# Optimization experiments

Hardware: AMD Instinct MI355X
Metric: run time of the kernel (lower is better)

The kernel has to match this reference:

```python
import jax, jax.numpy as jnp
import numpy as np

N = 100000   # nodes
E = 1600000  # edges
F = 64       # input node features
H = 64       # hidden dim
G = 512      # graphs in batch


def setup_inputs() -> dict:
    key = jax.random.key(0)
    ks = jax.random.split(key, 10)
    x = jax.random.normal(ks[0], (N, F), dtype=jnp.float32)
    edge_index = jax.random.randint(ks[1], (2, E), 0, N, dtype=jnp.int32)
    batch = jnp.sort(jax.random.randint(ks[2], (N,), 0, G, dtype=jnp.int32))
    s = 1.0 / np.sqrt(H)
    W1 = jax.random.normal(ks[3], (F, H), dtype=jnp.float32) * s
    b1 = jnp.zeros((H,), jnp.float32)
    W2 = jax.random.normal(ks[4], (H, H), dtype=jnp.float32) * s
    b2 = jnp.zeros((H,), jnp.float32)
    W3 = jax.random.normal(ks[5], (H, H), dtype=jnp.float32) * s
    b3 = jnp.zeros((H,), jnp.float32)
    return {"x": x, "edge_index": edge_index, "batch": batch,
            "W1": W1, "b1": b1, "W2": W2, "b2": b2, "W3": W3, "b3": b3}


def _gcn_conv(x, W, b, src, dst, dinv):
    # PyG GCNConv: h = x @ W; aggregate with sym-normalized adjacency incl. self-loops; + bias
    h = x @ W                                  # [N, H]
    norm = dinv[src] * dinv[dst]               # [E]
    agg = jax.ops.segment_sum(h[src] * norm[:, None], dst, num_segments=N)
    agg = agg + h * (dinv * dinv)[:, None]     # self-loop contribution
    return agg + b


def reference(x, edge_index, batch, W1, b1, W2, b2, W3, b3):
    src, dst = edge_index[0], edge_index[1]
    # degree with self-loops (counted on dst, as in PyG)
    deg = jax.ops.segment_sum(jnp.ones((E,), x.dtype), dst, num_segments=N) + 1.0
    dinv = jax.lax.rsqrt(deg)
    h = jax.nn.relu(_gcn_conv(x, W1, b1, src, dst, dinv))
    h = jax.nn.relu(_gcn_conv(h, W2, b2, src, dst, dinv))
    h = _gcn_conv(h, W3, b3, src, dst, dinv)
    # global mean pool over graphs
    sums = jax.ops.segment_sum(h, batch, num_segments=G)          # [G, H]
    cnts = jax.ops.segment_sum(jnp.ones((N,), h.dtype), batch, num_segments=G)
    return sums / jnp.maximum(cnts, 1.0)[:, None]
```

## Files before the change

### kernel.cpp

```cpp
#include <hip/hip_runtime.h>

#define N_NODES 100000
#define N_EDGES 1600000
#define FDIM 64
#define NGRAPH 512
#define NB 782
#define NWG 1024
#define CHUNK 1563
#define DWG 64
#define DCHUNK ((N_NODES + DWG - 1) / DWG)
#define MAXD 128

__device__ __forceinline__ unsigned short f2bf(float v) {
    unsigned int x = __float_as_uint(v);
    x += 0x7FFF + ((x >> 16) & 1);
    return (unsigned short)(x >> 16);
}

__global__ void scan_block(const int* __restrict__ in, int* __restrict__ excl,
                           int* __restrict__ blocksums, int n) {
    __shared__ int lds[256];
    int t = threadIdx.x;
    int base = blockIdx.x * 1024 + t * 4;
    int v0 = (base     < n) ? in[base]     : 0;
    int v1 = (base + 1 < n) ? in[base + 1] : 0;
    int v2 = (base + 2 < n) ? in[base + 2] : 0;
    int v3 = (base + 3 < n) ? in[base + 3] : 0;
    int s = v0 + v1 + v2 + v3;
    lds[t] = s;
    __syncthreads();
    for (int off = 1; off < 256; off <<= 1) {
        int x = (t >= off) ? lds[t - off] : 0;
        __syncthreads();
        lds[t] += x;
        __syncthreads();
    }
    int thrExcl = lds[t] - s;
    if (t == 255) blocksums[blockIdx.x] = lds[255];
    if (base     < n) excl[base]     = thrExcl;
    if (base + 1 < n) excl[base + 1] = thrExcl + v0;
    if (base + 2 < n) excl[base + 2] = thrExcl + v0 + v1;
    if (base + 3 < n) excl[base + 3] = thrExcl + v0 + v1 + v2;
}

__global__ void scan_top2(int* __restrict__ blocksums, int nb, int* __restrict__ out, int n) {
    __shared__ int lds[256];
    int t = threadIdx.x;
    int base = t * 4;
    int v0 = (base     < nb) ? blocksums[base]     : 0;
    int v1 = (base + 1 < nb) ? blocksums[base + 1] : 0;
    int v2 = (base + 2 < nb) ? blocksums[base + 2] : 0;
    int v3 = (base + 3 < nb) ? blocksums[base + 3] : 0;
    int s = v0 + v1 + v2 + v3;
    lds[t] = s;
    __syncthreads();
    for (int off = 1; off < 256; off <<= 1) {
        int x = (t >= off) ? lds[t - off] : 0;
        __syncthreads();
        lds[t] += x;
        __syncthreads();
    }
    int excl = lds[t] - s;
    if (base     < nb) blocksums[base]     = excl;
    if (base + 1 < nb) blocksums[base + 1] = excl + v0;
    if (base + 2 < nb) blocksums[base + 2] = excl + v0 + v1;
    if (base + 3 < nb) blocksums[base + 3] = excl + v0 + v1 + v2;
    if (t == 255) out[n] = lds[255];
}

__global__ void scan_add(int* __restrict__ out, const int* __restrict__ blocksums, int n) {
    int i = blockIdx.x * blockDim.x + threadIdx.x;
    if (i < n) out[i] += blocksums[i >> 10];
}

__global__ __launch_bounds__(256) void hist_kernel(const int* __restrict__ dst,
                                                   int* __restrict__ hist, int E) {
    __shared__ int h[NB];
    int t = threadIdx.x, wg = blockIdx.x;
    for (int i = t; i < NB; i += 256) h[i] = 0;
    __syncthreads();
    int beg = wg * CHUNK, end = min(beg + CHUNK, E);
    for (int i = beg + t; i < end; i += 256) atomicAdd(&h[dst[i] >> 7], 1);
    __syncthreads();
    for (int i = t; i < NB; i += 256) hist[i * NWG + wg] = h[i];
}

__global__ __launch_bounds__(256) void bin_kernel(const int* __restrict__ src,
                                                  const int* __restrict__ dst,
                                                  const int* __restrict__ scannedH,
                                                  int* __restrict__ ebin, int E) {
    __shared__ int base[NB];
    __shared__ int cur[NB];
    int t = threadIdx.x, wg = blockIdx.x;
    for (int i = t; i < NB; i += 256) { base[i] = scannedH[i * NWG + wg]; cur[i] = 0; }
    __syncthreads();
    int beg = wg * CHUNK, end = min(beg + CHUNK, E);
    for (int i = beg + t; i < end; i += 256) {
        int d = dst[i];
        int b = d >> 7;
        int p = base[b] + atomicAdd(&cur[b], 1);
        ebin[p] = ((d & 127) << 17) | src[i];
    }
}

__global__ __launch_bounds__(256) void csr_sort2(const int* __restrict__ ebin,
                                                 const int* __restrict__ scannedH,
                                                 int* __restrict__ csr_src,
                                                 int* __restrict__ offsets,
                                                 float* __restrict__ dinv, int E) {
    __shared__ int cnt[128];
    __shared__ int seg[128];
    __shared__ int cur[128];
    __shared__ int buf[4352];
    int t = threadIdx.x, b = blockIdx.x;
    int nbase = b << 7;
    int nodes = min(128, N_NODES - nbase);
    int bstart = scannedH[b * NWG];
    int bend = (b == NB - 1) ? E : scannedH[(b + 1) * NWG];
    if (t < 128) cnt[t] = 0;
    __syncthreads();
    for (int i = bstart + t; i < bend; i += 256) atomicAdd(&cnt[ebin[i] >> 17], 1);
    __syncthreads();
    if (t < 128) seg[t] = cnt[t];
    __syncthreads();
    for (int off = 1; off < 128; off <<= 1) {
        int v = 0;
        if (t < 128 && t >= off) v = seg[t - off];
        __syncthreads();
        if (t < 128) seg[t] += v;
        __syncthreads();
    }
    if (t < nodes) {
        int excl = seg[t] - cnt[t];
        offsets[nbase + t] = bstart + excl;
        dinv[nbase + t] = rsqrtf((float)cnt[t] + 1.0f);
        cur[t] = excl;
    }
    if (b == 0 && t == 0) offsets[N_NODES] = E;
    __syncthreads();
    for (int i = bstart + t; i < bend; i += 256) {
        int v = ebin[i];
        int p = atomicAdd(&cur[v >> 17], 1);
        buf[p] = v & 0x1FFFF;
    }
    __syncthreads();
    int span = bend - bstart;
    for (int i = t; i < span; i += 256) csr_src[bstart + i] = buf[i];
}

__global__ __launch_bounds__(256) void histD_kernel(const int* __restrict__ offsets,
                                                    int* __restrict__ histD) {
    __shared__ int h[MAXD];
    int t = threadIdx.x, wg = blockIdx.x;
    if (t < MAXD) h[t] = 0;
    __syncthreads();
    int beg = wg * DCHUNK, end = min(beg + DCHUNK, N_NODES);
    for (int i = beg + t; i < end; i += 256) {
        int d = min(offsets[i + 1] - offsets[i], MAXD - 1);
        atomicAdd(&h[d], 1);
    }
    __syncthreads();
    if (t < MAXD) histD[t * DWG + wg] = h[t];
}

__global__ __launch_bounds__(256) void binD_kernel(const int* __restrict__ offsets,
                                                   const int* __restrict__ scannedD,
                                                   int* __restrict__ perm) {
    __shared__ int base[MAXD];
    __shared__ int cur[MAXD];
    int t = threadIdx.x, wg = blockIdx.x;
    if (t < MAXD) { base[t] = scannedD[t * DWG + wg]; cur[t] = 0; }
    __syncthreads();
    int beg = wg * DCHUNK, end = min(beg + DCHUNK, N_NODES);
    for (int i = beg + t; i < end; i += 256) {
        int d = min(offsets[i + 1] - offsets[i], MAXD - 1);
        int pos = base[d] + atomicAdd(&cur[d], 1);
        perm[pos] = i;
    }
}

__global__ __launch_bounds__(256) void gemm64(const float* __restrict__ X,
                                              const float* __restrict__ W,
                                              const float* __restrict__ dinv,
                                              unsigned short* __restrict__ Hout, int n) {
    __shared__ float Ws[64 * 68];
    __shared__ float Xs[64 * 68];
    int t = threadIdx.x;
    int r0 = blockIdx.x * 64;

    #pragma unroll
    for (int kk = 0; kk < 16; ++kk) {
        int idx = t + kk * 256;
        int r = idx >> 6, c = idx & 63;
        Ws[r * 68 + c] = W[idx];
        float v = (r0 + r < n) ? X[(size_t)(r0 + r) * FDIM + c] : 0.0f;
        Xs[c * 68 + r] = v;
    }
    __syncthreads();

    int rg = (t >> 4) << 2;
    int cg = (t & 15) << 2;
    float4 acc0 = {0, 0, 0, 0}, acc1 = {0, 0, 0, 0};
    float4 acc2 = {0, 0, 0, 0}, acc3 = {0, 0, 0, 0};

    #pragma unroll 8
    for (int k = 0; k < 64; ++k) {
        float4 xv = *(const float4*)&Xs[k * 68 + rg];
        float4 wv = *(const float4*)&Ws[k * 68 + cg];
        acc0.x += xv.x * wv.x; acc0.y += xv.x * wv.y; acc0.z += xv.x * wv.z; acc0.w += xv.x * wv.w;
        acc1.x += xv.y * wv.x; acc1.y += xv.y * wv.y; acc1.z += xv.y * wv.z; acc1.w += xv.y * wv.w;
        acc2.x += xv.z * wv.x; acc2.y += xv.z * wv.y; acc2.z += xv.z * wv.z; acc2.w += xv.z * wv.w;
        acc3.x += xv.w * wv.x; acc3.y += xv.w * wv.y; acc3.z += xv.w * wv.z; acc3.w += xv.w * wv.w;
    }

    float4 accs[4] = {acc0, acc1, acc2, acc3};
    #pragma unroll
    for (int i = 0; i < 4; ++i) {
        int row = r0 + rg + i;
        if (row < n) {
            float sc = dinv[row];
            unsigned int u0 = (unsigned int)f2bf(accs[i].x * sc) | ((unsigned int)f2bf(accs[i].y * sc) << 16);
            unsigned int u1 = (unsigned int)f2bf(accs[i].z * sc) | ((unsigned int)f2bf(accs[i].w * sc) << 16);
            *(uint2*)&Hout[(size_t)row * FDIM + cg] = make_uint2(u0, u1);
        }
    }
}

__global__ __launch_bounds__(256) void gather_pn(const unsigned short* __restrict__ hs,
                                                 const int* __restrict__ csr_src,
                                                 const int* __restrict__ offsets,
                                                 const int* __restrict__ perm,
                                                 const float* __restrict__ dinv,
                                                 const float* __restrict__ bias,
                                                 float* __restrict__ outb,
                                                 int n, int do_relu) {
    int slot = (blockIdx.x * 256 + threadIdx.x) >> 3;
    int p = threadIdx.x & 7;
    if (slot >= n) return;
    int node = perm[slot];
    int beg = offsets[node], end = offsets[node + 1];

    float a0 = 0, a1 = 0, a2 = 0, a3 = 0, a4 = 0, a5 = 0, a6 = 0, a7 = 0;
    int k = beg;
    for (; k + 3 < end; k += 4) {
        int s0 = csr_src[k], s1 = csr_src[k + 1], s2 = csr_src[k + 2], s3 = csr_src[k + 3];
        uint4 v0 = *(const uint4*)(hs + ((size_t)s0 << 6) + (p << 3));
        uint4 v1 = *(const uint4*)(hs + ((size_t)s1 << 6) + (p << 3));
        uint4 v2 = *(const uint4*)(hs + ((size_t)s2 << 6) + (p << 3));
        uint4 v3 = *(const uint4*)(hs + ((size_t)s3 << 6) + (p << 3));
        a0 += __uint_as_float(v0.x << 16); a1 += __uint_as_float(v0.x & 0xFFFF0000u);
        a2 += __uint_as_float(v0.y << 16); a3 += __uint_as_float(v0.y & 0xFFFF0000u);
        a4 += __uint_as_float(v0.z << 16); a5 += __uint_as_float(v0.z & 0xFFFF0000u);
        a6 += __uint_as_float(v0.w << 16); a7 += __uint_as_float(v0.w & 0xFFFF0000u);
        a0 += __uint_as_float(v1.x << 16); a1 += __uint_as_float(v1.x & 0xFFFF0000u);
        a2 += __uint_as_float(v1.y << 16); a3 += __uint_as_float(v1.y & 0xFFFF0000u);
        a4 += __uint_as_float(v1.z << 16); a5 += __uint_as_float(v1.z & 0xFFFF0000u);
        a6 += __uint_as_float(v1.w << 16); a7 += __uint_as_float(v1.w & 0xFFFF0000u);
        a0 += __uint_as_float(v2.x << 16); a1 += __uint_as_float(v2.x & 0xFFFF0000u);
        a2 += __uint_as_float(v2.y << 16); a3 += __uint_as_float(v2.y & 0xFFFF0000u);
        a4 += __uint_as_float(v2.z << 16); a5 += __uint_as_float(v2.z & 0xFFFF0000u);
        a6 += __uint_as_float(v2.w << 16); a7 += __uint_as_float(v2.w & 0xFFFF0000u);
        a0 += __uint_as_float(v3.x << 16); a1 += __uint_as_float(v3.x & 0xFFFF0000u);
        a2 += __uint_as_float(v3.y << 16); a3 += __uint_as_float(v3.y & 0xFFFF0000u);
        a4 += __uint_as_float(v3.z << 16); a5 += __uint_as_float(v3.z & 0xFFFF0000u);
        a6 += __uint_as_float(v3.w << 16); a7 += __uint_as_float(v3.w & 0xFFFF0000u);
    }
    for (; k < end; ++k) {
        int s0 = csr_src[k];
        uint4 v0 = *(const uint4*)(hs + ((size_t)s0 << 6) + (p << 3));
        a0 += __uint_as_float(v0.x << 16); a1 += __uint_as_float(v0.x & 0xFFFF0000u);
        a2 += __uint_as_float(v0.y << 16); a3 += __uint_as_float(v0.y & 0xFFFF0000u);
        a4 += __uint_as_float(v0.z << 16); a5 += __uint_as_float(v0.z & 0xFFFF0000u);
        a6 += __uint_as_float(v0.w << 16); a7 += __uint_as_float(v0.w & 0xFFFF0000u);
    }
    uint4 sv = *(const uint4*)(hs + ((size_t)node << 6) + (p << 3));
    float dd = dinv[node];
    int fb = p << 3;
    const float4* bp = (const float4*)(bias + fb);
    float4 bv0 = bp[0], bv1 = bp[1];
    float o0 = dd * (a0 + __uint_as_float(sv.x << 16))        + bv0.x;
    float o1 = dd * (a1 + __uint_as_float(sv.x & 0xFFFF0000u)) + bv0.y;
    float o2 = dd * (a2 + __uint_as_float(sv.y << 16))        + bv0.z;
    float o3 = dd * (a3 + __uint_as_float(sv.y & 0xFFFF0000u)) + bv0.w;
    float o4 = dd * (a4 + __uint_as_float(sv.z << 16))        + bv1.x;
    float o5 = dd * (a5 + __uint_as_float(sv.z & 0xFFFF0000u)) + bv1.y;
    float o6 = dd * (a6 + __uint_as_float(sv.w << 16))        + bv1.z;
    float o7 = dd * (a7 + __uint_as_float(sv.w & 0xFFFF0000u)) + bv1.w;
    if (do_relu) {
        o0 = fmaxf(o0, 0.0f); o1 = fmaxf(o1, 0.0f); o2 = fmaxf(o2, 0.0f); o3 = fmaxf(o3, 0.0f);
        o4 = fmaxf(o4, 0.0f); o5 = fmaxf(o5, 0.0f); o6 = fmaxf(o6, 0.0f); o7 = fmaxf(o7, 0.0f);
    }
    float4* op = (float4*)(outb + (size_t)node * FDIM + fb);
    op[0] = make_float4(o0, o1, o2, o3);
    op[1] = make_float4(o4, o5, o6, o7);
}

__global__ void gstart_kernel(const int* __restrict__ batch, int* __restrict__ gstart, int n) {
    int g = blockIdx.x * blockDim.x + threadIdx.x;
    if (g > NGRAPH) return;
    if (g == NGRAPH) { gstart[NGRAPH] = n; return; }
    int lo = 0, hi = n;
    while (lo < hi) {
        int mid = (lo + hi) >> 1;
        if (batch[mid] < g) lo = mid + 1; else hi = mid;
    }
    gstart[g] = lo;
}

__global__ __launch_bounds__(256) void pool2(const float* __restrict__ h,
                                             const int* __restrict__ gstart,
                                             float* __restrict__ out) {
    __shared__ float red[4][64];
    int g = blockIdx.x;
    int beg = gstart[g], end = gstart[g + 1];
    int w = threadIdx.x >> 6, lane = threadIdx.x & 63;
    float acc = 0.0f;
    for (int i = beg + w; i < end; i += 4)
        acc += h[(size_t)i * FDIM + lane];
    red[w][lane] = acc;
    __syncthreads();
    if (w == 0) {
        float tot = red[0][lane] + red[1][lane] + red[2][lane] + red[3][lane];
        float cnt = (float)(end - beg);
        out[(size_t)g * FDIM + lane] = tot / fmaxf(cnt, 1.0f);
    }
}

extern "C" void kernel_launch(void* const* d_in, const int* in_sizes, int n_in,
                              void* d_out, int out_size, void* d_ws, size_t ws_size,
                              hipStream_t stream) {
    const float* x     = (const float*)d_in[0];
    const int*   ei    = (const int*)d_in[1];
    const int*   batch = (const int*)d_in[2];
    const float* W1    = (const float*)d_in[3];
    const float* b1    = (const float*)d_in[4];
    const float* W2    = (const float*)d_in[5];
    const float* b2    = (const float*)d_in[6];
    const float* W3    = (const float*)d_in[7];
    const float* b3    = (const float*)d_in[8];
    float* out = (float*)d_out;

    const int N = N_NODES, E = N_EDGES;
    const int* src = ei;
    const int* dst = ei + E;

    char* ws = (char*)d_ws;
    float*          dinv    = (float*)         (ws + 0);
    int*            offsets = (int*)           (ws + 400128);
    int*            csr_src = (int*)           (ws + 800256);
    float*          bufA    = (float*)         (ws + 7200384);
    unsigned short* hbf     = (unsigned short*)(ws + 32800384);
    int*            gstart  = (int*)           (ws + 45600384);
    int*            perm    = (int*)           (ws + 45602560);
    int*            scannedD= (int*)           (ws + 46002688);
    int*            blocksumsD=(int*)          (ws + 46035584);
    int* scannedH   = (int*)(ws + 7200384);
    int* blocksumsH = (int*)(ws + 10403584);
    int* ebin       = (int*)(ws + 10407936);

    hist_kernel<<<NWG, 256, 0, stream>>>(dst, scannedH, E);
    const int nH = NB * NWG;
    const int nScanH = (nH + 1023) / 1024;
    scan_block<<<nScanH, 256, 0, stream>>>(scannedH, scannedH, blocksumsH, nH);
    scan_top2<<<1, 256, 0, stream>>>(blocksumsH, nScanH, scannedH, nH);
    scan_add<<<(nH + 255) / 256, 256, 0, stream>>>(scannedH, blocksumsH, nH);
    bin_kernel<<<NWG, 256, 0, stream>>>(src, dst, scannedH, ebin, E);
    csr_sort2<<<NB, 256, 0, stream>>>(ebin, scannedH, csr_src, offsets, dinv, E);

    histD_kernel<<<DWG, 256, 0, stream>>>(offsets, scannedD);
    const int nD = MAXD * DWG;
    const int nScanD = (nD + 1023) / 1024;
    scan_block<<<nScanD, 256, 0, stream>>>(scannedD, scannedD, blocksumsD, nD);
    scan_top2<<<1, 256, 0, stream>>>(blocksumsD, nScanD, scannedD, nD);
    scan_add<<<(nD + 255) / 256, 256, 0, stream>>>(scannedD, blocksumsD, nD);
    binD_kernel<<<DWG, 256, 0, stream>>>(offsets, scannedD, perm);

    gstart_kernel<<<3, 256, 0, stream>>>(batch, gstart, N);

    const int gemmGrid   = (N + 63) / 64;
    const int gatherGrid = (N * 8 + 255) / 256;

    gemm64<<<gemmGrid, 256, 0, stream>>>(x, W1, dinv, hbf, N);
    gather_pn<<<gatherGrid, 256, 0, stream>>>(hbf, csr_src, offsets, perm, dinv, b1, bufA, N, 1);

    gemm64<<<gemmGrid, 256, 0, stream>>>(bufA, W2, dinv, hbf, N);
    gather_pn<<<gatherGrid, 256, 0, stream>>>(hbf, csr_src, offsets, perm, dinv, b2, bufA, N, 1);

    gemm64<<<gemmGrid, 256, 0, stream>>>(bufA, W3, dinv, hbf, N);
    gather_pn<<<gatherGrid, 256, 0, stream>>>(hbf, csr_src, offsets, perm, dinv, b3, bufA, N, 0);

    pool2<<<NGRAPH, 256, 0, stream>>>(bufA, gstart, out);
}
```

Before: 274.9 us.

## Halve binning workgroups, transpose histogram for coalesced access, single-kernel degree scan

Cuts the binning workgroups from 1024 to 512 with larger chunks. Per-workgroup histograms are now written row-major and coalesced, and tiled transposes move them to and from the bin-major layout the scan needs. The degree-histogram scan becomes one single-workgroup kernel in place of three launches, and bin_kernel handles two edges per thread. This trades uncoalesced strided histogram writes and reads, plus extra launches, for two added transpose kernels and fewer workgroups doing the atomic binning.

Measured after the change: 272.1 us. No clear change (-1.0%).

```diff
diff --git a/kernel.cpp b/kernel.cpp
--- a/kernel.cpp
+++ b/kernel.cpp
@@ -5,8 +5,9 @@
 #define FDIM 64
 #define NGRAPH 512
 #define NB 782
-#define NWG 1024
-#define CHUNK 1563
+#define NBP 784
+#define NWG 512
+#define CHUNK 3125
 #define DWG 64
 #define DCHUNK ((N_NODES + DWG - 1) / DWG)
 #define MAXD 128
@@ -43,7 +44,7 @@
     if (base + 3 < n) excl[base + 3] = thrExcl + v0 + v1 + v2;
 }
 
-__global__ void scan_top2(int* __restrict__ blocksums, int nb, int* __restrict__ out, int n) {
+__global__ void scan_top2(int* __restrict__ blocksums, int nb) {
     __shared__ int lds[256];
     int t = threadIdx.x;
     int base = t * 4;
@@ -65,7 +66,6 @@
     if (base + 1 < nb) blocksums[base + 1] = excl + v0;
     if (base + 2 < nb) blocksums[base + 2] = excl + v0 + v1;
     if (base + 3 < nb) blocksums[base + 3] = excl + v0 + v1 + v2;
-    if (t == 255) out[n] = lds[255];
 }
 
 __global__ void scan_add(int* __restrict__ out, const int* __restrict__ blocksums, int n) {
@@ -73,8 +73,55 @@
     if (i < n) out[i] += blocksums[i >> 10];
 }
 
+__global__ __launch_bounds__(256) void scan_single(int* __restrict__ data, int n) {
+    __shared__ int lds[256];
+    int t = threadIdx.x;
+    int loc[32];
+    int base = t * 32;
+    int s = 0;
+    #pragma unroll
+    for (int j = 0; j < 32; ++j) { loc[j] = (base + j < n) ? data[base + j] : 0; s += loc[j]; }
+    lds[t] = s;
+    __syncthreads();
+    for (int off = 1; off < 256; off <<= 1) {
+        int x = (t >= off) ? lds[t - off] : 0;
+        __syncthreads();
+        lds[t] += x;
+        __syncthreads();
+    }
+    int run = lds[t] - s;
+    #pragma unroll
+    for (int j = 0; j < 32; ++j) {
+        int v = loc[j];
+        if (base + j < n) data[base + j] = run;
+        run += v;
+    }
+}
+
+__global__ __launch_bounds__(256) void transpose_k(const int* __restrict__ src, int* __restrict__ dst,
+                                                   int R, int C, int spitch, int dpitch) {
+    __shared__ int tile[32][33];
+    int tilesC = (C + 31) >> 5;
+    int bx = blockIdx.x % tilesC;
+    int by = blockIdx.x / tilesC;
+    int tx = threadIdx.x & 31, ty = threadIdx.x >> 5;
+    int c = bx * 32 + tx;
+    #pragma unroll
+    for (int j = 0; j < 32; j += 8) {
+        int r = by * 32 + ty + j;
+        if (r < R && c < C) tile[ty + j][tx] = src[r * spitch + c];
+    }
+    __syncthreads();
+    int rT = by * 32 + tx;
+    #pragma unroll
+    for (int j = 0; j < 32; j += 8) {
+        int cT = bx * 32 + ty + j;
+        if (cT < C && rT < R) dst[cT * dpitch + rT] = tile[tx][ty + j];
+    }
+}
+
 __global__ __launch_bounds__(256) void hist_kernel(const int* __restrict__ dst,
-                                                   int* __restrict__ hist, int E) {
+                                                   int* __restrict__ histWG, int E) {
     __shared__ int h[NB];
     int t = threadIdx.x, wg = blockIdx.x;
     for (int i = t; i < NB; i += 256) h[i] = 0;
@@ -82,29 +129,35 @@
     int beg = wg * CHUNK, end = min(beg + CHUNK, E);
     for (int i = beg + t; i < end; i += 256) atomicAdd(&h[dst[i] >> 7], 1);
     __syncthreads();
-    for (int i = t; i < NB; i += 256) hist[i * NWG + wg] = h[i];
+    for (int i = t; i < NB; i += 256) histWG[wg * NBP + i] = h[i];
 }
 
 __global__ __launch_bounds__(256) void bin_kernel(const int* __restrict__ src,
                                                   const int* __restrict__ dst,
-                                                  const int* __restrict__ scannedH,
+                                                  const int* __restrict__ baseWG,
                                                   int* __restrict__ ebin, int E) {
     __shared__ int base[NB];
     __shared__ int cur[NB];
     int t = threadIdx.x, wg = blockIdx.x;
-    for (int i = t; i < NB; i += 256) { base[i] = scannedH[i * NWG + wg]; cur[i] = 0; }
+    for (int i = t; i < NB; i += 256) { base[i] = baseWG[wg * NBP + i]; cur[i] = 0; }
     __syncthreads();
     int beg = wg * CHUNK, end = min(beg + CHUNK, E);
-    for (int i = beg + t; i < end; i += 256) {
-        int d = dst[i];
-        int b = d >> 7;
-        int p = base[b] + atomicAdd(&cur[b], 1);
-        ebin[p] = ((d & 127) << 17) | src[i];
+    for (int i = beg + t * 2; i < end; i += 512) {
+        int d0 = dst[i], s0 = src[i];
+        int b0 = d0 >> 7;
+        int p0 = base[b0] + atomicAdd(&cur[b0], 1);
+        ebin[p0] = ((d0 & 127) << 17) | s0;
+        if (i + 1 < end) {
+            int d1 = dst[i + 1], s1 = src[i + 1];
+            int b1 = d1 >> 7;
+            int p1 = base[b1] + atomicAdd(&cur[b1], 1);
+            ebin[p1] = ((d1 & 127) << 17) | s1;
+        }
     }
 }
 
 __global__ __launch_bounds__(256) void csr_sort2(const int* __restrict__ ebin,
-                                                 const int* __restrict__ scannedH,
+                                                 const int* __restrict__ scannedT,
                                                  int* __restrict__ csr_src,
                                                  int* __restrict__ offsets,
                                                  float* __restrict__ dinv, int E) {
@@ -115,8 +168,8 @@
     int t = threadIdx.x, b = blockIdx.x;
     int nbase = b << 7;
     int nodes = min(128, N_NODES - nbase);
-    int bstart = scannedH[b * NWG];
-    int bend = (b == NB - 1) ? E : scannedH[(b + 1) * NWG];
+    int bstart = scannedT[b * NWG];
+    int bend = (b == NB - 1) ? E : scannedT[(b + 1) * NWG];
     if (t < 128) cnt[t] = 0;
     __syncthreads();
     for (int i = bstart + t; i < bend; i += 256) atomicAdd(&cnt[ebin[i] >> 17], 1);
@@ -353,26 +406,30 @@
     int*            gstart  = (int*)           (ws + 45600384);
     int*            perm    = (int*)           (ws + 45602560);
     int*            scannedD= (int*)           (ws + 46002688);
-    int*            blocksumsD=(int*)          (ws + 46035584);
-    int* scannedH   = (int*)(ws + 7200384);
-    int* blocksumsH = (int*)(ws + 10403584);
-    int* ebin       = (int*)(ws + 10407936);
-
-    hist_kernel<<<NWG, 256, 0, stream>>>(dst, scannedH, E);
+    int* histT      = (int*)(ws + 7200384);
+    int* blocksumsH = (int*)(ws + 8803328);
+    int* histWG     = (int*)(ws + 8805376);
+    int* ebin       = (int*)(ws + 10411520);
+
+    hist_kernel<<<NWG, 256, 0, stream>>>(dst, histWG, E);
+    {
+        int tilesC = (NB + 31) / 32, tilesR = (NWG + 31) / 32;
+        transpose_k<<<tilesC * tilesR, 256, 0, stream>>>(histWG, histT, NWG, NB, NBP, NWG);
+    }
     const int nH = NB * NWG;
     const int nScanH = (nH + 1023) / 1024;
-    scan_block<<<nScanH, 256, 0, stream>>>(scannedH, scannedH, blocksumsH, nH);
-    scan_top2<<<1, 256, 0, stream>>>(blocksumsH, nScanH, scannedH, nH);
-    scan_add<<<(nH + 255) / 256, 256, 0, stream>>>(scannedH, blocksumsH, nH);
-    bin_kernel<<<NWG, 256, 0, stream>>>(src, dst, scannedH, ebin, E);
-    csr_sort2<<<NB, 256, 0, stream>>>(ebin, scannedH, csr_src, offsets, dinv, E);
+    scan_block<<<nScanH, 256, 0, stream>>>(histT, histT, blocksumsH, nH);
+    scan_top2<<<1, 256, 0, stream>>>(blocksumsH, nScanH);
+    scan_add<<<(nH + 255) / 256, 256, 0, stream>>>(histT, blocksumsH, nH);
+    {
+        int tilesC = (NWG + 31) / 32, tilesR = (NB + 31) / 32;
+        transpose_k<<<tilesC * tilesR, 256, 0, stream>>>(histT, histWG, NB, NWG, NWG, NBP);
+    }
+    bin_kernel<<<NWG, 256, 0, stream>>>(src, dst, histWG, ebin, E);
+    csr_sort2<<<NB, 256, 0, stream>>>(ebin, histT, csr_src, offsets, dinv, E);
 
     histD_kernel<<<DWG, 256, 0, stream>>>(offsets, scannedD);
-    const int nD = MAXD * DWG;
-    const int nScanD = (nD + 1023) / 1024;
-    scan_block<<<nScanD, 256, 0, stream>>>(scannedD, scannedD, blocksumsD, nD);
-    scan_top2<<<1, 256, 0, stream>>>(blocksumsD, nScanD, scannedD, nD);
-    scan_add<<<(nD + 255) / 256, 256, 0, stream>>>(scannedD, blocksumsD, nD);
+    scan_single<<<1, 256, 0, stream>>>(scannedD, MAXD * DWG);
     binD_kernel<<<DWG, 256, 0, stream>>>(offsets, scannedD, perm);
 
     gstart_kernel<<<3, 256, 0, stream>>>(batch, gstart, N);
```
